# Kernel optimization log

Measured on AMD Instinct MI355X. Metric: run time of the kernel, lower is better.

The kernel has to match this reference:

```python
import jax, jax.numpy as jnp
import numpy as np

H = 8            # num_heads
WIN = 128        # num_windows (sliding-window half-width)
B, T, C = 2, 4096, 512


def setup_inputs() -> dict:
    key = jax.random.key(0)
    k1, k2, k3 = jax.random.split(key, 3)
    x = jax.random.normal(k1, (B, T, C), dtype=jnp.float32)
    W_qkv = jax.random.normal(k2, (C, 3 * C), dtype=jnp.float32) * (C ** -0.5)
    W_out = jax.random.normal(k3, (C, C), dtype=jnp.float32) * (C ** -0.5)
    b_out = jnp.zeros((C,), dtype=jnp.float32)
    return {"x": x, "W_qkv": W_qkv, "W_out": W_out, "b_out": b_out}


def reference(x, W_qkv, W_out, b_out):
    Bx, Tx, Cx = x.shape
    hd = Cx // H
    scale = hd ** -0.5
    # qkv projection -> [B, T, 3, H, hd]
    qkv = (x @ W_qkv).reshape(Bx, Tx, 3, H, hd)
    q, k, v = qkv[:, :, 0], qkv[:, :, 1], qkv[:, :, 2]  # each [B, T, H, hd]
    # attention scores [B, H, T, T]
    scores = jnp.einsum('bihd,bjhd->bhij', q, k) * scale
    idx = jnp.arange(Tx)
    band = jnp.abs(idx[:, None] - idx[None, :]) <= WIN  # [T, T] bool
    scores = jnp.where(band[None, None], scores, jnp.float32(-jnp.inf))
    attn = jax.nn.softmax(scores, axis=-1)
    # dropout is identity in eval mode (p handled by config; omitted)
    out = jnp.einsum('bhij,bjhd->bihd', attn, v).reshape(Bx, Tx, Cx)
    return out @ W_out + b_out
```

## Files before the change

### kernel.cpp

```cpp
#include <hip/hip_runtime.h>
#include <stdint.h>

typedef unsigned short ushort_t;
typedef __attribute__((ext_vector_type(8))) __bf16 bf16x8;
typedef __attribute__((ext_vector_type(8))) unsigned short ushortx8;
typedef __attribute__((ext_vector_type(4))) float floatx4;
typedef __attribute__((ext_vector_type(4))) unsigned int uint4v;

__device__ inline ushort_t f2bf(float f) {
  union { float f; unsigned u; } v; v.f = f;
  unsigned r = v.u + 0x7FFFu + ((v.u >> 16) & 1u);
  return (ushort_t)(r >> 16);
}

__device__ inline floatx4 mfma16(bf16x8 a, bf16x8 b, floatx4 c) {
  return __builtin_amdgcn_mfma_f32_16x16x32_bf16(a, b, c, 0, 0, 0);
}

__device__ inline void gload_lds16(const ushort_t* g, ushort_t* l) {
  __builtin_amdgcn_global_load_lds((__attribute__((address_space(1))) void*)(void*)(g),
                                   (__attribute__((address_space(3))) void*)(l),
                                   16, 0, 0);
}

__global__ __launch_bounds__(256)
void k_prep(const float* __restrict__ x, ushort_t* __restrict__ xb,
            const float* __restrict__ Wqkv, ushort_t* __restrict__ wqkvT,
            const float* __restrict__ Wout, ushort_t* __restrict__ woutT) {
  int bx = blockIdx.x, tid = threadIdx.x;
  if (bx < 4096) {
    int i = (bx * 256 + tid) * 4;
    float4 v = *(const float4*)(x + i);
    ushort4 o;
    o.x = f2bf(v.x); o.y = f2bf(v.y); o.z = f2bf(v.z); o.w = f2bf(v.w);
    *(ushort4*)(xb + i) = o;
    return;
  }
  __shared__ float tile[32][33];
  const float* src; ushort_t* dst; int N, id;
  if (bx < 4096 + 768) { id = bx - 4096; src = Wqkv; dst = wqkvT; N = 1536; }
  else                 { id = bx - 4864; src = Wout; dst = woutT; N = 512;  }
  int k0 = (id & 15) * 32, n0 = (id >> 4) * 32;
  int c = tid & 31, r0 = tid >> 5;
#pragma unroll
  for (int i = 0; i < 4; ++i) {
    int r = r0 + i * 8;
    tile[r][c] = src[(size_t)(k0 + r) * N + n0 + c];
  }
  __syncthreads();
#pragma unroll
  for (int i = 0; i < 4; ++i) {
    int r = r0 + i * 8;
    dst[(size_t)(n0 + r) * 512 + k0 + c] = f2bf(tile[c][r]);
  }
}

__global__ __launch_bounds__(256)
void k_gemm1(const ushort_t* __restrict__ A, const ushort_t* __restrict__ Bt,
             ushort_t* __restrict__ qd, ushort_t* __restrict__ kd,
             ushort_t* __restrict__ vtd) {
  __shared__ __align__(16) ushort_t smem[17408];
  ushort_t* As = smem;
  ushort_t* Bs = smem + 8192;
  const int tid = threadIdx.x;
  const int w = tid >> 6, l = tid & 63;
  const int lr = l & 15, lq = l >> 4;
  const int m0 = blockIdx.x * 128, n0 = blockIdx.y * 128;
  const int wm = w >> 1, wn = w & 1;

  floatx4 acc[4][4];
#pragma unroll
  for (int i = 0; i < 4; ++i)
#pragma unroll
    for (int j = 0; j < 4; ++j) acc[i][j] = (floatx4)0.0f;

  for (int k0 = 0; k0 < 512; k0 += 64) {
#pragma unroll
    for (int i = 0; i < 8; ++i) {
      int idx = w * 8 + i;
      if (idx < 16) {
        int blk = idx >> 1, half = idx & 1;
        gload_lds16(A + (size_t)(m0 + blk * 16 + lr) * 512 + k0 + half * 32 + lq * 8,
                    &As[blk * 1024 + half * 512]);
      } else {
        int j = idx - 16, blk = j >> 1, half = j & 1;
        gload_lds16(Bt + (size_t)(n0 + blk * 16 + lr) * 512 + k0 + half * 32 + lq * 8,
                    &Bs[blk * 1024 + half * 512]);
      }
    }
    __syncthreads();
#pragma unroll
    for (int half = 0; half < 2; ++half) {
      bf16x8 af[4], bfr[4];
#pragma unroll
      for (int i = 0; i < 4; ++i)
        af[i] = *(const bf16x8*)&As[(wm * 4 + i) * 1024 + half * 512 + l * 8];
#pragma unroll
      for (int j = 0; j < 4; ++j)
        bfr[j] = *(const bf16x8*)&Bs[(wn * 4 + j) * 1024 + half * 512 + l * 8];
#pragma unroll
      for (int i = 0; i < 4; ++i)
#pragma unroll
        for (int j = 0; j < 4; ++j) acc[i][j] = mfma16(af[i], bfr[j], acc[i][j]);
    }
    __syncthreads();
  }

  if (blockIdx.y < 8) {
#pragma unroll
    for (int i = 0; i < 4; ++i)
#pragma unroll
      for (int j = 0; j < 4; ++j) {
        int col = wn * 64 + j * 16 + lr;
#pragma unroll
        for (int r = 0; r < 4; ++r) {
          int row = wm * 64 + i * 16 + lq * 4 + r;
          smem[row * 136 + col] = f2bf(acc[i][j][r]);
        }
      }
    __syncthreads();
#pragma unroll
    for (int p = 0; p < 8; ++p) {
      int row = p * 16 + (tid >> 4), c8 = (tid & 15) * 8;
      ushortx8 vv = *(const ushortx8*)&smem[row * 136 + c8];
      int n = n0 + c8;
      ushort_t* dst = (n >> 9) ? kd : qd;
      int h = (n >> 6) & 7, d = n & 63;
      int m = m0 + row, b = m >> 12, t = m & 4095;
      *(ushortx8*)&dst[(((size_t)(b * 8 + h)) * 4096 + t) * 64 + d] = vv;
    }
  } else {
#pragma unroll
    for (int i = 0; i < 4; ++i)
#pragma unroll
      for (int j = 0; j < 4; ++j) {
        int dcol = wn * 64 + j * 16 + lr;
        int trow = wm * 64 + i * 16 + lq * 4;
        ushort4 pv;
        pv.x = f2bf(acc[i][j][0]); pv.y = f2bf(acc[i][j][1]);
        pv.z = f2bf(acc[i][j][2]); pv.w = f2bf(acc[i][j][3]);
        *(ushort4*)&smem[dcol * 136 + trow] = pv;
      }
    __syncthreads();
#pragma unroll
    for (int p = 0; p < 8; ++p) {
      int row = p * 16 + (tid >> 4), c8 = (tid & 15) * 8;
      ushortx8 vv = *(const ushortx8*)&smem[row * 136 + c8];
      int n = n0 + row, h = (n >> 6) & 7, d = n & 63;
      int m = m0 + c8, b = m >> 12, t = m & 4095;
      *(ushortx8*)&vtd[(((size_t)(b * 8 + h)) * 64 + d) * 4096 + t] = vv;
    }
  }
}

__global__ __launch_bounds__(256)
void k_gemm2(const ushort_t* __restrict__ A, const ushort_t* __restrict__ Bt,
             float* __restrict__ outf, const float* __restrict__ bias) {
  __shared__ __align__(16) char smemc[33792];
  ushort_t* As = (ushort_t*)smemc;
  ushort_t* Bs = (ushort_t*)(smemc + 8192);
  float* Cs = (float*)smemc;
  const int tid = threadIdx.x;
  const int w = tid >> 6, l = tid & 63;
  const int lr = l & 15, lq = l >> 4;
  const int m0 = blockIdx.x * 64, n0 = blockIdx.y * 128;
  const int wm = w >> 1, wn = w & 1;

  floatx4 acc[2][4];
#pragma unroll
  for (int i = 0; i < 2; ++i)
#pragma unroll
    for (int j = 0; j < 4; ++j) acc[i][j] = (floatx4)0.0f;

  for (int k0 = 0; k0 < 512; k0 += 64) {
#pragma unroll
    for (int i = 0; i < 6; ++i) {
      int idx = w * 6 + i;
      if (idx < 8) {
        int blk = idx >> 1, half = idx & 1;
        gload_lds16(A + (size_t)(m0 + blk * 16 + lr) * 512 + k0 + half * 32 + lq * 8,
                    &As[blk * 1024 + half * 512]);
      } else {
        int j = idx - 8, blk = j >> 1, half = j & 1;
        gload_lds16(Bt + (size_t)(n0 + blk * 16 + lr) * 512 + k0 + half * 32 + lq * 8,
                    &Bs[blk * 1024 + half * 512]);
      }
    }
    __syncthreads();
#pragma unroll
    for (int half = 0; half < 2; ++half) {
      bf16x8 af[2], bfr[4];
#pragma unroll
      for (int i = 0; i < 2; ++i)
        af[i] = *(const bf16x8*)&As[(wm * 2 + i) * 1024 + half * 512 + l * 8];
#pragma unroll
      for (int j = 0; j < 4; ++j)
        bfr[j] = *(const bf16x8*)&Bs[(wn * 4 + j) * 1024 + half * 512 + l * 8];
#pragma unroll
      for (int i = 0; i < 2; ++i)
#pragma unroll
        for (int j = 0; j < 4; ++j) acc[i][j] = mfma16(af[i], bfr[j], acc[i][j]);
    }
    __syncthreads();
  }

#pragma unroll
  for (int i = 0; i < 2; ++i)
#pragma unroll
    for (int j = 0; j < 4; ++j) {
      int col = wn * 64 + j * 16 + lr;
      float bv = bias[n0 + col];
#pragma unroll
      for (int r = 0; r < 4; ++r) {
        int row = wm * 32 + i * 16 + lq * 4 + r;
        Cs[row * 132 + col] = acc[i][j][r] + bv;
      }
    }
  __syncthreads();
#pragma unroll
  for (int p = 0; p < 4; ++p) {
    int row = p * 16 + (tid >> 4), c = (tid & 15) * 8;
    float4 v0 = *(const float4*)&Cs[row * 132 + c];
    float4 v1 = *(const float4*)&Cs[row * 132 + c + 4];
    float* op = &outf[(size_t)(m0 + row) * 512 + n0 + c];
    *(float4*)op = v0;
    *(float4*)(op + 4) = v1;
  }
}

__global__ __launch_bounds__(256)
void k_attn(const ushort_t* __restrict__ qa, const ushort_t* __restrict__ ka,
            const ushort_t* __restrict__ vta, ushort_t* __restrict__ ao) {
  __shared__ __align__(16) ushort_t S[20 * 1024];
  const int tid = threadIdx.x, w = tid >> 6, l = tid & 63;
  const int lr = l & 15, lq = l >> 4;
  const int g = blockIdx.x;
  const int xcd = g & 7, j = g >> 3;
  const int bh = xcd * 2 + (j & 1);
  const int qt0 = (j >> 1) * 64;
  const int qrow = qt0 + w * 16;

  const ushort_t* kbase = ka + (size_t)bh * 4096 * 64;
#pragma unroll
  for (int i = 0; i < 10; ++i) {
    int idx = w * 10 + i, blk = idx >> 1, half = idx & 1;
    int row = qt0 - 128 + blk * 16 + lr;
    row = min(max(row, 0), 4095);
    gload_lds16(kbase + (size_t)row * 64 + half * 32 + lq * 8, &S[blk * 1024 + half * 512]);
  }

  const ushort_t* qp = qa + ((size_t)bh * 4096 + qrow + lr) * 64 + lq * 8;
  bf16x8 qf0 = *(const bf16x8*)qp;
  bf16x8 qf1 = *(const bf16x8*)(qp + 32);

  __syncthreads();

  const float Cc = 0.125f * 1.4426950408889634f;
  uint2 pk[18];
  pk[17].x = 0u; pk[17].y = 0u;
  float ps = 0.f;
#pragma unroll
  for (int kt = 0; kt < 17; ++kt) {
    const ushort_t* kp = &S[(w + kt) * 1024 + l * 8];
    bf16x8 kf0 = *(const bf16x8*)kp;
    bf16x8 kf1 = *(const bf16x8*)(kp + 512);
    floatx4 s = (floatx4)0.0f;
    s = mfma16(kf0, qf0, s);
    s = mfma16(kf1, qf1, s);
    float p[4];
#pragma unroll
    for (int r = 0; r < 4; ++r) {
      int r_rel = kt * 16 + lq * 4 + r;
      int kj = qrow - 128 + r_rel;
      bool ok = (kj >= 0) && (kj < 4096) && (r_rel >= lr) && (r_rel - lr <= 256);
      float e = ok ? exp2f(s[r] * Cc) : 0.f;
      ps += e;
      p[r] = e;
    }
    pk[kt].x = (unsigned)f2bf(p[0]) | ((unsigned)f2bf(p[1]) << 16);
    pk[kt].y = (unsigned)f2bf(p[2]) | ((unsigned)f2bf(p[3]) << 16);
  }

  ps += __shfl_xor(ps, 16, 64);
  ps += __shfl_xor(ps, 32, 64);
  float inv = __builtin_amdgcn_rcpf(ps);
  float invr[4];
#pragma unroll
  for (int r = 0; r < 4; ++r) invr[r] = __shfl(inv, lq * 4 + r, 64);

  __syncthreads();

  const ushort_t* vbase = vta + (size_t)bh * 64 * 4096;
#pragma unroll
  for (int i = 0; i < 10; ++i) {
    int t = w * 10 + i, kt2 = t >> 2, nt = t & 3;
    int d = nt * 16 + lr;
    int key = qt0 - 128 + kt2 * 32 + lq * 8;
    key = min(max(key, 0), 4088);
    gload_lds16(vbase + (size_t)d * 4096 + key, &S[t * 512]);
  }

  const int srcA = ((l >> 4) & 1) * 32 + lr;
  const int srcB = srcA + 16;
  const bool selhi = (l & 32) != 0;
  bf16x8 pu9[9];
#pragma unroll
  for (int kk = 0; kk < 9; ++kk) {
    unsigned e0 = __shfl(pk[2 * kk].x, srcA, 64);
    unsigned e1 = __shfl(pk[2 * kk].y, srcA, 64);
    unsigned e2 = __shfl(pk[2 * kk].x, srcB, 64);
    unsigned e3 = __shfl(pk[2 * kk].y, srcB, 64);
    unsigned o0 = __shfl(pk[2 * kk + 1].x, srcA, 64);
    unsigned o1 = __shfl(pk[2 * kk + 1].y, srcA, 64);
    unsigned o2 = __shfl(pk[2 * kk + 1].x, srcB, 64);
    unsigned o3 = __shfl(pk[2 * kk + 1].y, srcB, 64);
    union { uint4v u; bf16x8 b; } pu;
    pu.u[0] = selhi ? o0 : e0;
    pu.u[1] = selhi ? o1 : e1;
    pu.u[2] = selhi ? o2 : e2;
    pu.u[3] = selhi ? o3 : e3;
    pu9[kk] = pu.b;
  }

  __syncthreads();

  floatx4 oacc[4];
#pragma unroll
  for (int nt = 0; nt < 4; ++nt) oacc[nt] = (floatx4)0.0f;
#pragma unroll
  for (int kk = 0; kk < 9; ++kk) {
    int keyrel = w * 16 + kk * 32 + lq * 8;
    keyrel = min(keyrel, 312);
    int kt2 = keyrel >> 5, seg = (keyrel >> 3) & 3;
    const ushort_t* vsp = &S[kt2 * 2048 + seg * 128 + lr * 8];
#pragma unroll
    for (int nt = 0; nt < 4; ++nt) {
      bf16x8 vf = *(const bf16x8*)(vsp + nt * 512);
      oacc[nt] = mfma16(pu9[kk], vf, oacc[nt]);
    }
  }

  __syncthreads();

#pragma unroll
  for (int nt = 0; nt < 4; ++nt)
#pragma unroll
    for (int r = 0; r < 4; ++r)
      S[(w * 16 + lq * 4 + r) * 72 + nt * 16 + lr] = f2bf(oacc[nt][r] * invr[r]);
  __syncthreads();

  int b = bh >> 3, h = bh & 7;
#pragma unroll
  for (int p = 0; p < 2; ++p) {
    int row = p * 32 + (tid >> 3), c8 = (tid & 7) * 8;
    ushortx8 vv = *(const ushortx8*)&S[row * 72 + c8];
    *(ushortx8*)&ao[((size_t)(b * 4096 + qt0 + row)) * 512 + h * 64 + c8] = vv;
  }
}

extern "C" void kernel_launch(void* const* d_in, const int* in_sizes, int n_in,
                              void* d_out, int out_size, void* d_ws, size_t ws_size,
                              hipStream_t stream) {
  const float* x    = (const float*)d_in[0];
  const float* Wqkv = (const float*)d_in[1];
  const float* Wout = (const float*)d_in[2];
  const float* bout = (const float*)d_in[3];
  float* out = (float*)d_out;
  char* ws = (char*)d_ws;
  const size_t MB = 1024 * 1024;

  ushort_t* xb    = (ushort_t*)(ws);
  ushort_t* wqkvT = (ushort_t*)(ws + 8 * MB);
  ushort_t* woutT = (ushort_t*)(ws + 9 * MB + MB/2);
  ushort_t* q     = (ushort_t*)(ws + 10 * MB);
  ushort_t* k     = (ushort_t*)(ws + 18 * MB);
  ushort_t* vt    = (ushort_t*)(ws + 26 * MB);
  ushort_t* ao    = xb;

  k_prep<<<5120, 256, 0, stream>>>(x, xb, Wqkv, wqkvT, Wout, woutT);
  k_gemm1<<<dim3(64, 12), 256, 0, stream>>>(xb, wqkvT, q, k, vt);
  k_attn<<<1024, 256, 0, stream>>>(q, k, vt, ao);
  k_gemm2<<<dim3(128, 4), 256, 0, stream>>>(ao, woutT, out, bout);
}
```

Measured before the change: 142.8 us.

## Load GEMM operands directly from global into registers, drop LDS staging

Both projection GEMMs stop staging A/B tiles in shared memory through global_load_lds with barriers. Each wave now loads its MFMA fragments straight from global memory into registers and relies on the L1/L2 caches for reuse across waves. The output GEMM also moves to 64x64 tiles with twice as many blocks, to improve occupancy and parallelism. This removes the LDS round trip and the per-iteration __syncthreads, at the cost of redundant global loads and less explicit data reuse.

```diff
diff --git a/kernel.cpp b/kernel.cpp
--- a/kernel.cpp
+++ b/kernel.cpp
@@ -60,50 +60,32 @@
              ushort_t* __restrict__ qd, ushort_t* __restrict__ kd,
              ushort_t* __restrict__ vtd) {
   __shared__ __align__(16) ushort_t smem[17408];
-  ushort_t* As = smem;
-  ushort_t* Bs = smem + 8192;
   const int tid = threadIdx.x;
   const int w = tid >> 6, l = tid & 63;
   const int lr = l & 15, lq = l >> 4;
   const int m0 = blockIdx.x * 128, n0 = blockIdx.y * 128;
   const int wm = w >> 1, wn = w & 1;
 
+  const ushort_t* Ab = A + (size_t)(m0 + wm * 64 + lr) * 512 + lq * 8;
+  const ushort_t* Bb = Bt + (size_t)(n0 + wn * 64 + lr) * 512 + lq * 8;
+
   floatx4 acc[4][4];
 #pragma unroll
   for (int i = 0; i < 4; ++i)
 #pragma unroll
     for (int j = 0; j < 4; ++j) acc[i][j] = (floatx4)0.0f;
 
-  for (int k0 = 0; k0 < 512; k0 += 64) {
-#pragma unroll
-    for (int i = 0; i < 8; ++i) {
-      int idx = w * 8 + i;
-      if (idx < 16) {
-        int blk = idx >> 1, half = idx & 1;
-        gload_lds16(A + (size_t)(m0 + blk * 16 + lr) * 512 + k0 + half * 32 + lq * 8,
-                    &As[blk * 1024 + half * 512]);
-      } else {
-        int j = idx - 16, blk = j >> 1, half = j & 1;
-        gload_lds16(Bt + (size_t)(n0 + blk * 16 + lr) * 512 + k0 + half * 32 + lq * 8,
-                    &Bs[blk * 1024 + half * 512]);
-      }
-    }
-    __syncthreads();
-#pragma unroll
-    for (int half = 0; half < 2; ++half) {
-      bf16x8 af[4], bfr[4];
-#pragma unroll
-      for (int i = 0; i < 4; ++i)
-        af[i] = *(const bf16x8*)&As[(wm * 4 + i) * 1024 + half * 512 + l * 8];
-#pragma unroll
-      for (int j = 0; j < 4; ++j)
-        bfr[j] = *(const bf16x8*)&Bs[(wn * 4 + j) * 1024 + half * 512 + l * 8];
-#pragma unroll
-      for (int i = 0; i < 4; ++i)
-#pragma unroll
-        for (int j = 0; j < 4; ++j) acc[i][j] = mfma16(af[i], bfr[j], acc[i][j]);
-    }
-    __syncthreads();
+#pragma unroll 2
+  for (int k0 = 0; k0 < 512; k0 += 32) {
+    bf16x8 af[4], bfr[4];
+#pragma unroll
+    for (int i = 0; i < 4; ++i) af[i] = *(const bf16x8*)(Ab + (size_t)i * 16 * 512 + k0);
+#pragma unroll
+    for (int j = 0; j < 4; ++j) bfr[j] = *(const bf16x8*)(Bb + (size_t)j * 16 * 512 + k0);
+#pragma unroll
+    for (int i = 0; i < 4; ++i)
+#pragma unroll
+      for (int j = 0; j < 4; ++j) acc[i][j] = mfma16(af[i], bfr[j], acc[i][j]);
   }
 
   if (blockIdx.y < 8) {
@@ -156,75 +138,53 @@
 __global__ __launch_bounds__(256)
 void k_gemm2(const ushort_t* __restrict__ A, const ushort_t* __restrict__ Bt,
              float* __restrict__ outf, const float* __restrict__ bias) {
-  __shared__ __align__(16) char smemc[33792];
-  ushort_t* As = (ushort_t*)smemc;
-  ushort_t* Bs = (ushort_t*)(smemc + 8192);
-  float* Cs = (float*)smemc;
+  __shared__ __align__(16) float Cs[64 * 68];
   const int tid = threadIdx.x;
   const int w = tid >> 6, l = tid & 63;
   const int lr = l & 15, lq = l >> 4;
-  const int m0 = blockIdx.x * 64, n0 = blockIdx.y * 128;
+  const int m0 = blockIdx.x * 64, n0 = blockIdx.y * 64;
   const int wm = w >> 1, wn = w & 1;
 
-  floatx4 acc[2][4];
+  const ushort_t* Ab = A + (size_t)(m0 + wm * 32 + lr) * 512 + lq * 8;
+  const ushort_t* Bb = Bt + (size_t)(n0 + wn * 32 + lr) * 512 + lq * 8;
+
+  floatx4 acc[2][2];
 #pragma unroll
   for (int i = 0; i < 2; ++i)
 #pragma unroll
-    for (int j = 0; j < 4; ++j) acc[i][j] = (floatx4)0.0f;
-
-  for (int k0 = 0; k0 < 512; k0 += 64) {
-#pragma unroll
-    for (int i = 0; i < 6; ++i) {
-      int idx = w * 6 + i;
-      if (idx < 8) {
-        int blk = idx >> 1, half = idx & 1;
-        gload_lds16(A + (size_t)(m0 + blk * 16 + lr) * 512 + k0 + half * 32 + lq * 8,
-                    &As[blk * 1024 + half * 512]);
-      } else {
-        int j = idx - 8, blk = j >> 1, half = j & 1;
-        gload_lds16(Bt + (size_t)(n0 + blk * 16 + lr) * 512 + k0 + half * 32 + lq * 8,
-                    &Bs[blk * 1024 + half * 512]);
-      }
-    }
-    __syncthreads();
-#pragma unroll
-    for (int half = 0; half < 2; ++half) {
-      bf16x8 af[2], bfr[4];
-#pragma unroll
-      for (int i = 0; i < 2; ++i)
-        af[i] = *(const bf16x8*)&As[(wm * 2 + i) * 1024 + half * 512 + l * 8];
-#pragma unroll
-      for (int j = 0; j < 4; ++j)
-        bfr[j] = *(const bf16x8*)&Bs[(wn * 4 + j) * 1024 + half * 512 + l * 8];
-#pragma unroll
-      for (int i = 0; i < 2; ++i)
-#pragma unroll
-        for (int j = 0; j < 4; ++j) acc[i][j] = mfma16(af[i], bfr[j], acc[i][j]);
-    }
-    __syncthreads();
+    for (int j = 0; j < 2; ++j) acc[i][j] = (floatx4)0.0f;
+
+#pragma unroll 4
+  for (int k0 = 0; k0 < 512; k0 += 32) {
+    bf16x8 af[2], bfr[2];
+#pragma unroll
+    for (int i = 0; i < 2; ++i) af[i] = *(const bf16x8*)(Ab + (size_t)i * 16 * 512 + k0);
+#pragma unroll
+    for (int j = 0; j < 2; ++j) bfr[j] = *(const bf16x8*)(Bb + (size_t)j * 16 * 512 + k0);
+#pragma unroll
+    for (int i = 0; i < 2; ++i)
+#pragma unroll
+      for (int j = 0; j < 2; ++j) acc[i][j] = mfma16(af[i], bfr[j], acc[i][j]);
   }
 
 #pragma unroll
   for (int i = 0; i < 2; ++i)
 #pragma unroll
-    for (int j = 0; j < 4; ++j) {
-      int col = wn * 64 + j * 16 + lr;
+    for (int j = 0; j < 2; ++j) {
+      int col = wn * 32 + j * 16 + lr;
       float bv = bias[n0 + col];
 #pragma unroll
       for (int r = 0; r < 4; ++r) {
         int row = wm * 32 + i * 16 + lq * 4 + r;
-        Cs[row * 132 + col] = acc[i][j][r] + bv;
+        Cs[row * 68 + col] = acc[i][j][r] + bv;
       }
     }
   __syncthreads();
 #pragma unroll
   for (int p = 0; p < 4; ++p) {
-    int row = p * 16 + (tid >> 4), c = (tid & 15) * 8;
-    float4 v0 = *(const float4*)&Cs[row * 132 + c];
-    float4 v1 = *(const float4*)&Cs[row * 132 + c + 4];
-    float* op = &outf[(size_t)(m0 + row) * 512 + n0 + c];
-    *(float4*)op = v0;
-    *(float4*)(op + 4) = v1;
+    int row = p * 16 + (tid >> 4), c = (tid & 15) * 4;
+    float4 v0 = *(const float4*)&Cs[row * 68 + c];
+    *(float4*)&outf[(size_t)(m0 + row) * 512 + n0 + c] = v0;
   }
 }
 
@@ -380,5 +340,5 @@
   k_prep<<<5120, 256, 0, stream>>>(x, xb, Wqkv, wqkvT, Wout, woutT);
   k_gemm1<<<dim3(64, 12), 256, 0, stream>>>(xb, wqkvT, q, k, vt);
   k_attn<<<1024, 256, 0, stream>>>(q, k, vt, ao);
-  k_gemm2<<<dim3(128, 4), 256, 0, stream>>>(ao, woutT, out, bout);
-}
+  k_gemm2<<<dim3(128, 8), 256, 0, stream>>>(ao, woutT, out, bout);
+}
```

Result: slower. 172.9 us (+21.0%).
